# Kernel optimization log

Measured on AMD Instinct MI355X. Metric: run time of the kernel, lower is better.

The kernel has to match this reference:

```python
import jax, jax.numpy as jnp
import numpy as np

L = 2      # shared recursion blocks
B = 2
T = 4096
D = 1024
H = 16
DH = D // H
F = 4096
K = 2048   # token-choice capacity (active tokens per sequence)
S = 0.02   # init scale


def setup_inputs() -> dict:
    key = jax.random.key(0)
    ks = jax.random.split(key, 8)
    return {
        "x": jax.random.normal(ks[0], (B, T, D), jnp.float32),
        "router_w": jax.random.normal(ks[1], (D,), jnp.float32) * S,
        "router_b": jnp.zeros((), jnp.float32),
        "ln1_w": jnp.ones((L, D), jnp.float32),
        "ln1_b": jnp.zeros((L, D), jnp.float32),
        "wqkv": jax.random.normal(ks[2], (L, D, 3 * D), jnp.float32) * S,
        "wo": jax.random.normal(ks[3], (L, D, D), jnp.float32) * S,
        "ln2_w": jnp.ones((L, D), jnp.float32),
        "ln2_b": jnp.zeros((L, D), jnp.float32),
        "w1": jax.random.normal(ks[4], (L, D, F), jnp.float32) * S,
        "w2": jax.random.normal(ks[5], (L, F, D), jnp.float32) * S,
        "k": K,
    }


def _ln(x, w, b):
    mu = x.mean(-1, keepdims=True)
    var = ((x - mu) ** 2).mean(-1, keepdims=True)
    return (x - mu) * jax.lax.rsqrt(var + 1e-5) * w + b


def _block(h, ln1w, ln1b, wqkv, wo, ln2w, ln2b, w1, w2):
    # pre-LN MHA + pre-LN MLP transformer block over the active token subset
    Bk, Kk, Dd = h.shape
    y = _ln(h, ln1w, ln1b)
    qkv = jnp.einsum("bkd,de->bke", y, wqkv)          # [B,K,3D]
    q, kk, v = jnp.split(qkv, 3, axis=-1)
    sh = lambda t: t.reshape(Bk, Kk, H, DH).transpose(0, 2, 1, 3)  # [B,H,K,DH]
    q, kk, v = sh(q), sh(kk), sh(v)
    scores = jnp.einsum("bhqd,bhkd->bhqk", q, kk) / jnp.sqrt(jnp.float32(DH))
    att = jax.nn.softmax(scores, axis=-1)
    o = jnp.einsum("bhqk,bhkd->bhqd", att, v).transpose(0, 2, 1, 3).reshape(Bk, Kk, Dd)
    h = h + jnp.einsum("bkd,de->bke", o, wo)
    y = _ln(h, ln2w, ln2b)
    h = h + jnp.einsum("bkf,fd->bkd", jax.nn.gelu(jnp.einsum("bkd,df->bkf", y, w1)), w2)
    return h


def reference(x, router_w, router_b, ln1_w, ln1_b, wqkv, wo, ln2_w, ln2_b, w1, w2, k):
    # --- token-choice router: per-token scalar logit, top-k capacity selection ---
    logits = jnp.einsum("btd,d->bt", x, router_w) + router_b       # [B,T]
    top_v, selected = jax.lax.top_k(logits, k)                     # [B,K]
    gate_w = jax.nn.sigmoid(top_v)[..., None]                      # [B,K,1]
    # --- gather active tokens (torch.gather along dim 1) ---
    top_k_x = jnp.take_along_axis(x, selected[..., None], axis=1)  # [B,K,D]
    # --- shared recursion blocks ---
    h = top_k_x
    for l in range(L):
        h = _block(h, ln1_w[l], ln1_b[l], wqkv[l], wo[l],
                   ln2_w[l], ln2_b[l], w1[l], w2[l])
    h_out = h * gate_w                                             # weighted gating
    # --- scatter_add back into the full sequence ---
    b_idx = jnp.arange(x.shape[0])[:, None]                        # [B,1]
    out = x.at[b_idx, selected].add(h_out)
    return out
```

## Files before the change

### kernel.cpp

```cpp
#include <hip/hip_runtime.h>
#include <cmath>

typedef __bf16 bf16;
typedef __bf16 bf16x2 __attribute__((ext_vector_type(2)));
typedef __bf16 bf16x4 __attribute__((ext_vector_type(4)));
typedef __bf16 bf16x8 __attribute__((ext_vector_type(8)));
typedef float  f32x4  __attribute__((ext_vector_type(4)));

#define AS1(p) ((const __attribute__((address_space(1))) void*)(p))
#define AS3(p) ((__attribute__((address_space(3))) void*)(p))

constexpr int Bc = 2, Tc = 4096, Dc = 1024, Hc = 16, Fc = 4096, Kc = 2048;

__global__ __launch_bounds__(256) void router_kernel(const float* __restrict__ x,
    const float* __restrict__ rw, const float* __restrict__ rb, float* __restrict__ logits,
    int* __restrict__ slot, int* __restrict__ sel, float* __restrict__ gate){
  int flat = blockIdx.x * 256 + threadIdx.x;
  if (flat < Bc * Tc) slot[flat] = -1;
  if (flat < Bc * Kc){ sel[flat] = flat & (Kc - 1); gate[flat] = 0.f; }
  int wv = threadIdx.x >> 6, lane = threadIdx.x & 63;
  int token = blockIdx.x * 4 + wv;
  const float* xr = x + (size_t)token * Dc;
  float s = 0.f;
#pragma unroll
  for (int i = 0; i < 16; i++){ int d = lane + i*64; s += xr[d] * rw[d]; }
#pragma unroll
  for (int m = 32; m; m >>= 1) s += __shfl_xor(s, m);
  if (lane == 0) logits[token] = s + rb[0];
}

__global__ __launch_bounds__(256) void topk_kernel(const float* __restrict__ logits,
    int* __restrict__ slot, int* __restrict__ sel, float* __restrict__ gate){
  __shared__ float lg[Tc];
  int b = blockIdx.x >> 7, seg = blockIdx.x & 127;
  const float* lb = logits + (size_t)b * Tc;
#pragma unroll
  for (int i = 0; i < 4; i++)
    *(float4*)&lg[(threadIdx.x + i*256)*4] = *(const float4*)&lb[(threadIdx.x + i*256)*4];
  __syncthreads();
  int t = seg * 32 + (threadIdx.x >> 3);
  int c = threadIdx.x & 7;
  float v = lg[t];
  int rank = 0;
#pragma unroll 4
  for (int j4 = c*128; j4 < c*128 + 128; j4++){
    float4 u4 = *(const float4*)&lg[j4*4];
    int j = j4*4;
    rank += (u4.x > v) || (u4.x == v && (j+0) < t);
    rank += (u4.y > v) || (u4.y == v && (j+1) < t);
    rank += (u4.z > v) || (u4.z == v && (j+2) < t);
    rank += (u4.w > v) || (u4.w == v && (j+3) < t);
  }
  rank += __shfl_xor(rank, 1);
  rank += __shfl_xor(rank, 2);
  rank += __shfl_xor(rank, 4);
  if (c == 0 && rank < Kc){
    sel [b*Kc + rank] = t;
    gate[b*Kc + rank] = 1.f / (1.f + expf(-v));
    slot[b*Tc + t] = rank;
  }
}

__global__ __launch_bounds__(256) void gather_kernel(const float* __restrict__ x,
    const int* __restrict__ sel, float* __restrict__ h){
  int row = blockIdx.x;
  int b = row >> 11;
  int t = sel[row];
  t = (t < 0) ? 0 : (t >= Tc ? Tc - 1 : t);
  const float* xr = x + ((size_t)b * Tc + t) * Dc;
  float* hr = h + (size_t)row * Dc;
  int d = threadIdx.x * 4;
  *(float4*)(hr + d) = *(const float4*)(xr + d);
}

__global__ __launch_bounds__(256) void ln_kernel(const float* __restrict__ h,
    const float* __restrict__ w, const float* __restrict__ bb, bf16* __restrict__ y){
  __shared__ float red[4], red2[4];
  int row = blockIdx.x, t = threadIdx.x;
  int wv = t >> 6, lane = t & 63;
  const float* hr = h + (size_t)row * Dc;
  float4 x4 = *(const float4*)(hr + t*4);
  float s = x4.x + x4.y + x4.z + x4.w;
#pragma unroll
  for (int m = 32; m; m >>= 1) s += __shfl_xor(s, m);
  if (lane == 0) red[wv] = s;
  __syncthreads();
  float mu = (red[0]+red[1]+red[2]+red[3]) * (1.f/Dc);
  float d0 = x4.x-mu, d1 = x4.y-mu, d2 = x4.z-mu, d3 = x4.w-mu;
  float q = d0*d0 + d1*d1 + d2*d2 + d3*d3;
#pragma unroll
  for (int m = 32; m; m >>= 1) q += __shfl_xor(q, m);
  if (lane == 0) red2[wv] = q;
  __syncthreads();
  float var = (red2[0]+red2[1]+red2[2]+red2[3]) * (1.f/Dc);
  float rs = rsqrtf(var + 1e-5f);
  bf16* yr = y + (size_t)row * Dc;
  int d = t * 4;
  float xv[4] = {x4.x, x4.y, x4.z, x4.w};
#pragma unroll
  for (int i = 0; i < 4; i++)
    yr[d+i] = (bf16)((xv[i]-mu) * rs * w[d+i] + bb[d+i]);
}

__device__ __forceinline__ void transpose_tile(const float* __restrict__ in,
    bf16* __restrict__ out, int R, int C, int bx, int by, bf16 (*tile)[72]){
  int c0 = bx * 64, r0 = by * 64;
  int t = threadIdx.x;
#pragma unroll
  for (int i = 0; i < 2; i++){
    int ch = t + i*256;
    int row = ch >> 3, col8 = (ch & 7) * 8;
    const float* src = in + (size_t)(r0+row)*C + c0 + col8;
    float4 a = *(const float4*)src;
    float4 b = *(const float4*)(src + 4);
    bf16x8 v;
    v[0]=(bf16)a.x; v[1]=(bf16)a.y; v[2]=(bf16)a.z; v[3]=(bf16)a.w;
    v[4]=(bf16)b.x; v[5]=(bf16)b.y; v[6]=(bf16)b.z; v[7]=(bf16)b.w;
    *(bf16x8*)&tile[row][col8] = v;
  }
  __syncthreads();
#pragma unroll
  for (int i = 0; i < 2; i++){
    int ch = t + i*256;
    int orow = ch >> 3, oc8 = (ch & 7) * 8;
    bf16x8 v;
#pragma unroll
    for (int j = 0; j < 8; j++) v[j] = tile[oc8+j][orow];
    *(bf16x8*)(out + (size_t)(c0+orow)*R + r0 + oc8) = v;
  }
}

__global__ __launch_bounds__(256) void transpose4_kernel(
    const float* __restrict__ wqkv, const float* __restrict__ wo,
    const float* __restrict__ w1,   const float* __restrict__ w2,
    bf16* __restrict__ wqkvT, bf16* __restrict__ woT,
    bf16* __restrict__ w1T,   bf16* __restrict__ w2T){
  __shared__ __attribute__((aligned(16))) bf16 tile[64][72];
  int id = blockIdx.x;
  if (id < 768)        transpose_tile(wqkv, wqkvT, Dc, 3*Dc, id % 48,        id / 48,        tile);
  else if (id < 1024){ int t = id - 768;  transpose_tile(wo, woT, Dc, Dc,   t % 16,         t / 16,         tile); }
  else if (id < 2048){ int t = id - 1024; transpose_tile(w1, w1T, Dc, Fc,   t % 64,         t / 64,         tile); }
  else               { int t = id - 2048; transpose_tile(w2, w2T, Fc, Dc,   t % 16,         t / 16,         tile); }
}

__device__ __forceinline__ float fast_gelu(float v){
  float u = exp2f(v * (1.f + 0.044715f*v*v) * -2.30220772f);
  return v * __builtin_amdgcn_rcpf(1.f + u);
}

__global__ __launch_bounds__(256) void gemm_bt_kernel(
    const bf16* __restrict__ A, const bf16* __restrict__ Bt,
    bf16* __restrict__ Cbf, float* __restrict__ Cf,
    int M, int N, int Kd, int mode)
{
  __shared__ __attribute__((aligned(16))) bf16 As[128*64];
  __shared__ __attribute__((aligned(16))) bf16 Bs[128*64];
  const int tid = threadIdx.x;
  const int wv = tid >> 6, lane = tid & 63;
  const int wm = wv & 1, wn = wv >> 1;
  const int quad = lane >> 4, l15 = lane & 15;
  const int m0 = blockIdx.y * 128, n0 = blockIdx.x * 128;
  f32x4 acc[4][4] = {};

  const int arow = tid >> 3;
  const int acol = ((tid & 7) ^ (arow & 7)) * 8;
  const bf16* Ag = A  + (size_t)(m0 + arow) * Kd + acol;
  const bf16* Bg = Bt + (size_t)(n0 + arow) * Kd + acol;
  char* AsB = (char*)As;
  char* BsB = (char*)Bs;
  const size_t rstep = (size_t)32 * Kd;

  const bf16* Ab = As + (size_t)(wm*64 + l15) * 64;
  const bf16* Bb = Bs + (size_t)(wn*64 + l15) * 64;
  const int rx = l15 & 7;

  for (int k0 = 0; k0 < Kd; k0 += 64){
    __syncthreads();
#pragma unroll
    for (int i = 0; i < 4; i++){
      __builtin_amdgcn_global_load_lds(AS1(Ag + i*rstep + k0), AS3(AsB + i*4096 + wv*1024), 16, 0, 0);
      __builtin_amdgcn_global_load_lds(AS1(Bg + i*rstep + k0), AS3(BsB + i*4096 + wv*1024), 16, 0, 0);
    }
    __syncthreads();
#pragma unroll
    for (int s = 0; s < 2; s++){
      const int ax = ((s*4 + quad) ^ rx) * 8;
      bf16x8 af[4], bfr[4];
#pragma unroll
      for (int mt = 0; mt < 4; mt++) af[mt]  = *(const bf16x8*)(Ab + mt*1024 + ax);
#pragma unroll
      for (int nt = 0; nt < 4; nt++) bfr[nt] = *(const bf16x8*)(Bb + nt*1024 + ax);
#pragma unroll
      for (int mt = 0; mt < 4; mt++)
#pragma unroll
        for (int nt = 0; nt < 4; nt++)
          acc[mt][nt] = __builtin_amdgcn_mfma_f32_16x16x32_bf16(af[mt], bfr[nt], acc[mt][nt], 0, 0, 0);
    }
  }
#pragma unroll
  for (int mt = 0; mt < 4; mt++){
    int rr0 = m0 + wm*64 + mt*16 + (lane>>4)*4;
#pragma unroll
    for (int nt = 0; nt < 4; nt++){
      int cc = n0 + wn*64 + nt*16 + (lane&15);
#pragma unroll
      for (int r = 0; r < 4; r++){
        float v = acc[mt][nt][r];
        size_t idx = (size_t)(rr0 + r) * N + cc;
        if (mode == 0)      Cbf[idx] = (bf16)v;
        else if (mode == 1) Cf[idx] += v;
        else                Cbf[idx] = (bf16)fast_gelu(v);
      }
    }
  }
}

__global__ __launch_bounds__(256) void gemm_bt64_kernel(
    const bf16* __restrict__ A, const bf16* __restrict__ Bt,
    bf16* __restrict__ Cbf, float* __restrict__ Cf,
    int M, int N, int Kd, int mode,
    const float* __restrict__ xg, const int* __restrict__ sel,
    const float* __restrict__ gatep, float* __restrict__ outp)
{
  __shared__ __attribute__((aligned(16))) bf16 As[128*64];
  __shared__ __attribute__((aligned(16))) bf16 Bs[64*64];
  const int tid = threadIdx.x;
  const int wv = tid >> 6, lane = tid & 63;
  const int wm = wv >> 1, wn = wv & 1;
  const int quad = lane >> 4, l15 = lane & 15;
  const int m0 = blockIdx.y * 128, n0 = blockIdx.x * 64;
  f32x4 acc[4][2] = {};

  const int arow = tid >> 3;
  const int acol = ((tid & 7) ^ (arow & 7)) * 8;
  const bf16* Ag = A  + (size_t)(m0 + arow) * Kd + acol;
  const bf16* Bg = Bt + (size_t)(n0 + arow) * Kd + acol;
  char* AsB = (char*)As;
  char* BsB = (char*)Bs;
  const size_t rstep = (size_t)32 * Kd;

  const bf16* Ab = As + (size_t)(wm*64 + l15) * 64;
  const bf16* Bb = Bs + (size_t)(wn*32 + l15) * 64;
  const int rx = l15 & 7;

  for (int k0 = 0; k0 < Kd; k0 += 64){
    __syncthreads();
#pragma unroll
    for (int i = 0; i < 4; i++)
      __builtin_amdgcn_global_load_lds(AS1(Ag + i*rstep + k0), AS3(AsB + i*4096 + wv*1024), 16, 0, 0);
#pragma unroll
    for (int i = 0; i < 2; i++)
      __builtin_amdgcn_global_load_lds(AS1(Bg + i*rstep + k0), AS3(BsB + i*4096 + wv*1024), 16, 0, 0);
    __syncthreads();
#pragma unroll
    for (int s = 0; s < 2; s++){
      const int ax = ((s*4 + quad) ^ rx) * 8;
      bf16x8 af[4], bfr[2];
#pragma unroll
      for (int mt = 0; mt < 4; mt++) af[mt]  = *(const bf16x8*)(Ab + mt*1024 + ax);
#pragma unroll
      for (int nt = 0; nt < 2; nt++) bfr[nt] = *(const bf16x8*)(Bb + nt*1024 + ax);
#pragma unroll
      for (int mt = 0; mt < 4; mt++)
#pragma unroll
        for (int nt = 0; nt < 2; nt++)
          acc[mt][nt] = __builtin_amdgcn_mfma_f32_16x16x32_bf16(af[mt], bfr[nt], acc[mt][nt], 0, 0, 0);
    }
  }
  if (mode == 3){
#pragma unroll
    for (int mt = 0; mt < 4; mt++){
      int rr0 = m0 + wm*64 + mt*16 + quad*4;
#pragma unroll
      for (int r = 0; r < 4; r++){
        int row = rr0 + r;
        int bb = row >> 11;
        int t  = sel[row];
        t = (t < 0) ? 0 : (t >= Tc ? Tc - 1 : t);
        float g = gatep[row];
        const size_t obase = ((size_t)bb * Tc + t) * (size_t)Dc;
#pragma unroll
        for (int nt = 0; nt < 2; nt++){
          int cc = n0 + wn*32 + nt*16 + l15;
          float hv = Cf[(size_t)row * N + cc] + acc[mt][nt][r];
          outp[obase + cc] = xg[obase + cc] + g * hv;
        }
      }
    }
    return;
  }
#pragma unroll
  for (int mt = 0; mt < 4; mt++){
    int rr0 = m0 + wm*64 + mt*16 + (lane>>4)*4;
#pragma unroll
    for (int nt = 0; nt < 2; nt++){
      int cc = n0 + wn*32 + nt*16 + (lane&15);
#pragma unroll
      for (int r = 0; r < 4; r++){
        float v = acc[mt][nt][r];
        size_t idx = (size_t)(rr0 + r) * N + cc;
        if (mode == 0)      Cbf[idx] = (bf16)v;
        else if (mode == 1) Cf[idx] += v;
        else                Cbf[idx] = (bf16)fast_gelu(v);
      }
    }
  }
}

__global__ __launch_bounds__(256) void flash_kernel(const bf16* __restrict__ qkv, bf16* __restrict__ o){
  __shared__ __attribute__((aligned(16))) bf16 Ks[64][72];
  __shared__ __attribute__((aligned(16))) bf16 Vt[64*64];
  __shared__ __attribute__((aligned(16))) bf16 Pt[4][64][16];
  const int tid = threadIdx.x, wv = tid >> 6, lane = tid & 63;
  const int quad = lane >> 4, l15 = lane & 15;
  const int bid = blockIdx.x;
  const int qt = bid & 31, hh = (bid >> 5) & 15, b = bid >> 9;
  const int q0 = qt * 64;
  const size_t base = (size_t)b * Kc * (3*Dc);
  const float SC2 = 0.125f * 1.44269504f;

  const int sp8 = (tid & 7) * 8;
  const int kr0 = tid >> 3, kr1 = kr0 + 32;
  const int vr0 = (tid >> 3) * 2;
  const int vg = vr0 >> 3, vlo = vr0 & 7, vsw = sp8 >> 3;

  bf16x8 qf[2];
  {
    const bf16* qr = qkv + base + (size_t)(q0 + wv*16 + l15)*(3*Dc) + hh*64 + quad*8;
    qf[0] = *(const bf16x8*)(qr);
    qf[1] = *(const bf16x8*)(qr + 32);
  }

  const bf16* kp0 = qkv + base + (size_t)kr0*(3*Dc) +   Dc + hh*64 + sp8;
  const bf16* kp1 = qkv + base + (size_t)kr1*(3*Dc) +   Dc + hh*64 + sp8;
  const bf16* vp0 = qkv + base + (size_t)vr0*(3*Dc) + 2*Dc + hh*64 + sp8;
  const bf16* vp1 = vp0 + 3*Dc;
  bf16x8 kpre0 = *(const bf16x8*)kp0;
  bf16x8 kpre1 = *(const bf16x8*)kp1;
  bf16x8 vpre0 = *(const bf16x8*)vp0;
  bf16x8 vpre1 = *(const bf16x8*)vp1;
  const int TSTRIDE = 64 * 3 * Dc;

  bf16x8 onesf;
#pragma unroll
  for (int j = 0; j < 8; j++) onesf[j] = (bf16)(l15 == 0 ? 1.f : 0.f);

  f32x4 oacc[4] = {};
  f32x4 oacc5 = {};
  float mrow[4];
#pragma unroll
  for (int r = 0; r < 4; r++) mrow[r] = -1e30f;

  for (int kt = 0; kt < 32; kt++){
    __syncthreads();
    *(bf16x8*)&Ks[kr0][sp8] = kpre0;
    *(bf16x8*)&Ks[kr1][sp8] = kpre1;
#pragma unroll
    for (int j = 0; j < 8; j++){
      bf16x2 pr; pr[0] = vpre0[j]; pr[1] = vpre1[j];
      *(bf16x2*)&Vt[(sp8 + j)*64 + ((vg ^ j ^ vsw) << 3) + vlo] = pr;
    }
    __syncthreads();
    if (kt < 31){
      kp0 += TSTRIDE; kp1 += TSTRIDE; vp0 += TSTRIDE; vp1 += TSTRIDE;
      kpre0 = *(const bf16x8*)kp0;
      kpre1 = *(const bf16x8*)kp1;
      vpre0 = *(const bf16x8*)vp0;
      vpre1 = *(const bf16x8*)vp1;
    }
    f32x4 sacc[4] = {};
    __builtin_amdgcn_s_setprio(1);
#pragma unroll
    for (int nt = 0; nt < 4; nt++)
#pragma unroll
      for (int s = 0; s < 2; s++){
        bf16x8 kf = *(const bf16x8*)&Ks[nt*16 + l15][s*32 + quad*8];
        sacc[nt] = __builtin_amdgcn_mfma_f32_16x16x32_bf16(qf[s], kf, sacc[nt], 0, 0, 0);
      }
    __builtin_amdgcn_s_setprio(0);
    float lm[4];
#pragma unroll
    for (int r = 0; r < 4; r++)
      lm[r] = fmaxf(fmaxf(sacc[0][r], sacc[1][r]), fmaxf(sacc[2][r], sacc[3][r]));
    bool ok = true;
#pragma unroll
    for (int r = 0; r < 4; r++) ok = ok && (lm[r] * SC2 <= mrow[r] + 8.f);
    if (!__all((int)ok)){
#pragma unroll
      for (int r = 0; r < 4; r++){
        float mx = lm[r];
#pragma unroll
        for (int m = 1; m < 16; m <<= 1) mx = fmaxf(mx, __shfl_xor(mx, m));
        float nm = fmaxf(mrow[r], mx * SC2);
        float alpha = exp2f(mrow[r] - nm);
        mrow[r] = nm;
#pragma unroll
        for (int nt = 0; nt < 4; nt++) oacc[nt][r] *= alpha;
        oacc5[r] *= alpha;
      }
    }
#pragma unroll
    for (int nt = 0; nt < 4; nt++){
      bf16x4 w;
#pragma unroll
      for (int r = 0; r < 4; r++) w[r] = (bf16)exp2f(fmaf(sacc[nt][r], SC2, -mrow[r]));
      *(bf16x4*)&Pt[wv][nt*16 + l15][quad*4] = w;
    }
    bf16x8 pf[2];
    {
      bf16x4 t00, t01, t10, t11;
      const bf16* pr0 = &Pt[wv][     quad*8][l15];
      const bf16* pr1 = &Pt[wv][32 + quad*8][l15];
      asm volatile("ds_read_b64_tr_b16 %0, %1"            : "=v"(t00) : "v"(AS3(pr0)) : "memory");
      asm volatile("ds_read_b64_tr_b16 %0, %1 offset:128" : "=v"(t01) : "v"(AS3(pr0)) : "memory");
      asm volatile("ds_read_b64_tr_b16 %0, %1"            : "=v"(t10) : "v"(AS3(pr1)) : "memory");
      asm volatile("ds_read_b64_tr_b16 %0, %1 offset:128" : "=v"(t11) : "v"(AS3(pr1)) : "memory");
      asm volatile("s_waitcnt lgkmcnt(0)" ::: "memory");
      __builtin_amdgcn_sched_barrier(0);
#pragma unroll
      for (int j = 0; j < 4; j++){
        pf[0][j] = t00[j]; pf[0][j+4] = t01[j];
        pf[1][j] = t10[j]; pf[1][j+4] = t11[j];
      }
    }
    __builtin_amdgcn_s_setprio(1);
#pragma unroll
    for (int nt = 0; nt < 4; nt++){
      int d = nt*16 + l15;
      int sw = (d & 7) ^ ((d >> 3) & 7);
#pragma unroll
      for (int s = 0; s < 2; s++){
        bf16x8 vf = *(const bf16x8*)&Vt[d*64 + (((s*4 + quad) ^ sw) << 3)];
        oacc[nt] = __builtin_amdgcn_mfma_f32_16x16x32_bf16(pf[s], vf, oacc[nt], 0, 0, 0);
      }
    }
    oacc5 = __builtin_amdgcn_mfma_f32_16x16x32_bf16(pf[0], onesf, oacc5, 0, 0, 0);
    oacc5 = __builtin_amdgcn_mfma_f32_16x16x32_bf16(pf[1], onesf, oacc5, 0, 0, 0);
    __builtin_amdgcn_s_setprio(0);
  }
#pragma unroll
  for (int r = 0; r < 4; r++){
    float l = __shfl(oacc5[r], lane & 48);
    float inv = __builtin_amdgcn_rcpf(l);
    int row = q0 + wv*16 + quad*4 + r;
#pragma unroll
    for (int nt = 0; nt < 4; nt++)
      o[((size_t)b*Kc + row)*Dc + hh*64 + nt*16 + l15] = (bf16)(oacc[nt][r] * inv);
  }
}

__global__ __launch_bounds__(256) void scatter_kernel(const float* __restrict__ x,
    const int* __restrict__ slot, float* __restrict__ out){
  int row = blockIdx.x;
  int sl = slot[row];
  if (sl >= 0 && sl < Kc) return;
  int d = threadIdx.x * 4;
  const float* xr = x + (size_t)row * Dc;
  float* orow = out + (size_t)row * Dc;
  *(float4*)(orow + d) = *(const float4*)(xr + d);
}

extern "C" void kernel_launch(void* const* d_in, const int* in_sizes, int n_in,
                              void* d_out, int out_size, void* d_ws, size_t ws_size,
                              hipStream_t stream)
{
  const float* x        = (const float*)d_in[0];
  const float* router_w = (const float*)d_in[1];
  const float* router_b = (const float*)d_in[2];
  const float* ln1_w    = (const float*)d_in[3];
  const float* ln1_b    = (const float*)d_in[4];
  const float* wqkv     = (const float*)d_in[5];
  const float* wo       = (const float*)d_in[6];
  const float* ln2_w    = (const float*)d_in[7];
  const float* ln2_b    = (const float*)d_in[8];
  const float* w1       = (const float*)d_in[9];
  const float* w2       = (const float*)d_in[10];
  float* out = (float*)d_out;

  char* ws = (char*)d_ws;
  if (ws_size < 84029440u) return;
  float* logits = (float*)(ws + 0);
  int*   slot   = (int*)  (ws + 36864);
  int*   sel    = (int*)  (ws + 73728);
  float* gate   = (float*)(ws + 94208);
  float* h      = (float*)(ws + 114688);
  bf16*  y      = (bf16*) (ws + 16896000);
  bf16*  big    = (bf16*) (ws + 25288704);
  bf16*  wqkvT  = (bf16*) (ws + 58847232);
  bf16*  woT    = (bf16*) (ws + 65142784);
  bf16*  w1T    = (bf16*) (ws + 67244032);
  bf16*  w2T    = (bf16*) (ws + 75636736);

  router_kernel<<<2048, 256, 0, stream>>>(x, router_w, router_b, logits, slot, sel, gate);
  topk_kernel<<<256, 256, 0, stream>>>(logits, slot, sel, gate);
  gather_kernel<<<4096, 256, 0, stream>>>(x, sel, h);

  for (int l = 0; l < 2; l++){
    transpose4_kernel<<<3072, 256, 0, stream>>>(
        wqkv + (size_t)l*Dc*3*Dc, wo + (size_t)l*Dc*Dc,
        w1 + (size_t)l*Dc*Fc,     w2 + (size_t)l*Fc*Dc,
        wqkvT, woT, w1T, w2T);

    ln_kernel<<<4096, 256, 0, stream>>>(h, ln1_w + l*Dc, ln1_b + l*Dc, y);
    gemm_bt_kernel<<<dim3(24,32), 256, 0, stream>>>(y, wqkvT, big, nullptr, 4096, 3*Dc, Dc, 0);
    flash_kernel<<<1024, 256, 0, stream>>>(big, y);
    gemm_bt64_kernel<<<dim3(16,32), 256, 0, stream>>>(y, woT, nullptr, h, 4096, Dc, Dc, 1,
                                                      nullptr, nullptr, nullptr, nullptr);
    ln_kernel<<<4096, 256, 0, stream>>>(h, ln2_w + l*Dc, ln2_b + l*Dc, y);
    gemm_bt_kernel<<<dim3(32,32), 256, 0, stream>>>(y, w1T, big, nullptr, 4096, Fc, Dc, 2);
    if (l == 0)
      gemm_bt64_kernel<<<dim3(16,32), 256, 0, stream>>>(big, w2T, nullptr, h, 4096, Dc, Fc, 1,
                                                        nullptr, nullptr, nullptr, nullptr);
    else
      gemm_bt64_kernel<<<dim3(16,32), 256, 0, stream>>>(big, w2T, nullptr, h, 4096, Dc, Fc, 3,
                                                        x, sel, gate, out);
  }

  scatter_kernel<<<8192, 256, 0, stream>>>(x, slot, out);
}
```

Before: 793.0 us.

## Double flash-attention KV tile to 128 and XCD-swizzle GEMM block order

The flash attention kernel now processes 128 keys per iteration instead of 64, with larger K, V-transposed and P shared-memory tiles. This halves the number of loop iterations and block-wide barriers and gives more MFMA work per synchronisation, at the cost of more LDS and registers per block, which may lower occupancy. Both GEMM kernels remap block IDs with an XCD-aware swizzle so that neighbouring tiles run on the same XCD and share its L2.

```diff
diff --git a/kernel.cpp b/kernel.cpp
--- a/kernel.cpp
+++ b/kernel.cpp
@@ -148,6 +148,10 @@
   return v * __builtin_amdgcn_rcpf(1.f + u);
 }
 
+__device__ __forceinline__ int xcd_swizzle(int id, int nwg){
+  return (id & 7) * (nwg >> 3) + (id >> 3);
+}
+
 __global__ __launch_bounds__(256) void gemm_bt_kernel(
     const bf16* __restrict__ A, const bf16* __restrict__ Bt,
     bf16* __restrict__ Cbf, float* __restrict__ Cf,
@@ -159,7 +163,9 @@
   const int wv = tid >> 6, lane = tid & 63;
   const int wm = wv & 1, wn = wv >> 1;
   const int quad = lane >> 4, l15 = lane & 15;
-  const int m0 = blockIdx.y * 128, n0 = blockIdx.x * 128;
+  const int nwg = gridDim.x * gridDim.y;
+  const int bid = xcd_swizzle(blockIdx.y * gridDim.x + blockIdx.x, nwg);
+  const int m0 = (bid / gridDim.x) * 128, n0 = (bid % gridDim.x) * 128;
   f32x4 acc[4][4] = {};
 
   const int arow = tid >> 3;
@@ -228,7 +234,9 @@
   const int wv = tid >> 6, lane = tid & 63;
   const int wm = wv >> 1, wn = wv & 1;
   const int quad = lane >> 4, l15 = lane & 15;
-  const int m0 = blockIdx.y * 128, n0 = blockIdx.x * 64;
+  const int nwg = gridDim.x * gridDim.y;
+  const int bid = xcd_swizzle(blockIdx.y * gridDim.x + blockIdx.x, nwg);
+  const int m0 = (bid / gridDim.x) * 128, n0 = (bid % gridDim.x) * 64;
   f32x4 acc[4][2] = {};
 
   const int arow = tid >> 3;
@@ -308,9 +316,9 @@
 }
 
 __global__ __launch_bounds__(256) void flash_kernel(const bf16* __restrict__ qkv, bf16* __restrict__ o){
-  __shared__ __attribute__((aligned(16))) bf16 Ks[64][72];
-  __shared__ __attribute__((aligned(16))) bf16 Vt[64*64];
-  __shared__ __attribute__((aligned(16))) bf16 Pt[4][64][16];
+  __shared__ __attribute__((aligned(16))) bf16 Ks[128][72];
+  __shared__ __attribute__((aligned(16))) bf16 Vt[128*64];
+  __shared__ __attribute__((aligned(16))) bf16 Pt[4][128][16];
   const int tid = threadIdx.x, wv = tid >> 6, lane = tid & 63;
   const int quad = lane >> 4, l15 = lane & 15;
   const int bid = blockIdx.x;
@@ -320,7 +328,7 @@
   const float SC2 = 0.125f * 1.44269504f;
 
   const int sp8 = (tid & 7) * 8;
-  const int kr0 = tid >> 3, kr1 = kr0 + 32;
+  const int kr0 = tid >> 3;
   const int vr0 = (tid >> 3) * 2;
   const int vg = vr0 >> 3, vlo = vr0 & 7, vsw = sp8 >> 3;
 
@@ -331,15 +339,18 @@
     qf[1] = *(const bf16x8*)(qr + 32);
   }
 
-  const bf16* kp0 = qkv + base + (size_t)kr0*(3*Dc) +   Dc + hh*64 + sp8;
-  const bf16* kp1 = qkv + base + (size_t)kr1*(3*Dc) +   Dc + hh*64 + sp8;
-  const bf16* vp0 = qkv + base + (size_t)vr0*(3*Dc) + 2*Dc + hh*64 + sp8;
-  const bf16* vp1 = vp0 + 3*Dc;
-  bf16x8 kpre0 = *(const bf16x8*)kp0;
-  bf16x8 kpre1 = *(const bf16x8*)kp1;
-  bf16x8 vpre0 = *(const bf16x8*)vp0;
-  bf16x8 vpre1 = *(const bf16x8*)vp1;
-  const int TSTRIDE = 64 * 3 * Dc;
+  const bf16* kp[4]; const bf16* vp[4];
+#pragma unroll
+  for (int i = 0; i < 4; i++)
+    kp[i] = qkv + base + (size_t)(kr0 + i*32)*(3*Dc) + Dc + hh*64 + sp8;
+  vp[0] = qkv + base + (size_t)(vr0     )*(3*Dc) + 2*Dc + hh*64 + sp8;
+  vp[1] = vp[0] + 3*Dc;
+  vp[2] = qkv + base + (size_t)(vr0 + 64)*(3*Dc) + 2*Dc + hh*64 + sp8;
+  vp[3] = vp[2] + 3*Dc;
+  bf16x8 kpre[4], vpre[4];
+#pragma unroll
+  for (int i = 0; i < 4; i++){ kpre[i] = *(const bf16x8*)kp[i]; vpre[i] = *(const bf16x8*)vp[i]; }
+  const int TSTRIDE = 128 * 3 * Dc;
 
   bf16x8 onesf;
 #pragma unroll
@@ -351,27 +362,31 @@
 #pragma unroll
   for (int r = 0; r < 4; r++) mrow[r] = -1e30f;
 
-  for (int kt = 0; kt < 32; kt++){
+  for (int kt = 0; kt < 16; kt++){
     __syncthreads();
-    *(bf16x8*)&Ks[kr0][sp8] = kpre0;
-    *(bf16x8*)&Ks[kr1][sp8] = kpre1;
+#pragma unroll
+    for (int i = 0; i < 4; i++)
+      *(bf16x8*)&Ks[kr0 + i*32][sp8] = kpre[i];
 #pragma unroll
     for (int j = 0; j < 8; j++){
-      bf16x2 pr; pr[0] = vpre0[j]; pr[1] = vpre1[j];
-      *(bf16x2*)&Vt[(sp8 + j)*64 + ((vg ^ j ^ vsw) << 3) + vlo] = pr;
+      bf16x2 pa; pa[0] = vpre[0][j]; pa[1] = vpre[1][j];
+      bf16x2 pb; pb[0] = vpre[2][j]; pb[1] = vpre[3][j];
+      *(bf16x2*)&Vt[(sp8 + j)*128 + (((vg    ) ^ j ^ vsw) << 3) + vlo] = pa;
+      *(bf16x2*)&Vt[(sp8 + j)*128 + (((vg + 8) ^ j ^ vsw) << 3) + vlo] = pb;
     }
     __syncthreads();
-    if (kt < 31){
-      kp0 += TSTRIDE; kp1 += TSTRIDE; vp0 += TSTRIDE; vp1 += TSTRIDE;
-      kpre0 = *(const bf16x8*)kp0;
-      kpre1 = *(const bf16x8*)kp1;
-      vpre0 = *(const bf16x8*)vp0;
-      vpre1 = *(const bf16x8*)vp1;
-    }
-    f32x4 sacc[4] = {};
+    if (kt < 15){
+#pragma unroll
+      for (int i = 0; i < 4; i++){
+        kp[i] += TSTRIDE; vp[i] += TSTRIDE;
+        kpre[i] = *(const bf16x8*)kp[i];
+        vpre[i] = *(const bf16x8*)vp[i];
+      }
+    }
+    f32x4 sacc[8] = {};
     __builtin_amdgcn_s_setprio(1);
 #pragma unroll
-    for (int nt = 0; nt < 4; nt++)
+    for (int nt = 0; nt < 8; nt++)
 #pragma unroll
       for (int s = 0; s < 2; s++){
         bf16x8 kf = *(const bf16x8*)&Ks[nt*16 + l15][s*32 + quad*8];
@@ -380,8 +395,11 @@
     __builtin_amdgcn_s_setprio(0);
     float lm[4];
 #pragma unroll
-    for (int r = 0; r < 4; r++)
-      lm[r] = fmaxf(fmaxf(sacc[0][r], sacc[1][r]), fmaxf(sacc[2][r], sacc[3][r]));
+    for (int r = 0; r < 4; r++){
+      float m0 = fmaxf(fmaxf(sacc[0][r], sacc[1][r]), fmaxf(sacc[2][r], sacc[3][r]));
+      float m1 = fmaxf(fmaxf(sacc[4][r], sacc[5][r]), fmaxf(sacc[6][r], sacc[7][r]));
+      lm[r] = fmaxf(m0, m1);
+    }
     bool ok = true;
 #pragma unroll
     for (int r = 0; r < 4; r++) ok = ok && (lm[r] * SC2 <= mrow[r] + 8.f);
@@ -400,28 +418,29 @@
       }
     }
 #pragma unroll
-    for (int nt = 0; nt < 4; nt++){
+    for (int nt = 0; nt < 8; nt++){
       bf16x4 w;
 #pragma unroll
       for (int r = 0; r < 4; r++) w[r] = (bf16)exp2f(fmaf(sacc[nt][r], SC2, -mrow[r]));
       *(bf16x4*)&Pt[wv][nt*16 + l15][quad*4] = w;
     }
-    bf16x8 pf[2];
+    bf16x8 pf[4];
     {
-      bf16x4 t00, t01, t10, t11;
-      const bf16* pr0 = &Pt[wv][     quad*8][l15];
-      const bf16* pr1 = &Pt[wv][32 + quad*8][l15];
-      asm volatile("ds_read_b64_tr_b16 %0, %1"            : "=v"(t00) : "v"(AS3(pr0)) : "memory");
-      asm volatile("ds_read_b64_tr_b16 %0, %1 offset:128" : "=v"(t01) : "v"(AS3(pr0)) : "memory");
-      asm volatile("ds_read_b64_tr_b16 %0, %1"            : "=v"(t10) : "v"(AS3(pr1)) : "memory");
-      asm volatile("ds_read_b64_tr_b16 %0, %1 offset:128" : "=v"(t11) : "v"(AS3(pr1)) : "memory");
+      bf16x4 tlo[4], thi[4];
+#pragma unroll
+      for (int s = 0; s < 4; s++){
+        const bf16* pr = &Pt[wv][s*32 + quad*8][l15];
+        asm volatile("ds_read_b64_tr_b16 %0, %1"            : "=v"(tlo[s]) : "v"(AS3(pr)) : "memory");
+        asm volatile("ds_read_b64_tr_b16 %0, %1 offset:128" : "=v"(thi[s]) : "v"(AS3(pr)) : "memory");
+      }
       asm volatile("s_waitcnt lgkmcnt(0)" ::: "memory");
       __builtin_amdgcn_sched_barrier(0);
 #pragma unroll
-      for (int j = 0; j < 4; j++){
-        pf[0][j] = t00[j]; pf[0][j+4] = t01[j];
-        pf[1][j] = t10[j]; pf[1][j+4] = t11[j];
-      }
+      for (int s = 0; s < 4; s++)
+#pragma unroll
+        for (int j = 0; j < 4; j++){
+          pf[s][j] = tlo[s][j]; pf[s][j+4] = thi[s][j];
+        }
     }
     __builtin_amdgcn_s_setprio(1);
 #pragma unroll
@@ -429,13 +448,14 @@
       int d = nt*16 + l15;
       int sw = (d & 7) ^ ((d >> 3) & 7);
 #pragma unroll
-      for (int s = 0; s < 2; s++){
-        bf16x8 vf = *(const bf16x8*)&Vt[d*64 + (((s*4 + quad) ^ sw) << 3)];
+      for (int s = 0; s < 4; s++){
+        bf16x8 vf = *(const bf16x8*)&Vt[d*128 + (((s*4 + quad) ^ sw) << 3)];
         oacc[nt] = __builtin_amdgcn_mfma_f32_16x16x32_bf16(pf[s], vf, oacc[nt], 0, 0, 0);
       }
     }
-    oacc5 = __builtin_amdgcn_mfma_f32_16x16x32_bf16(pf[0], onesf, oacc5, 0, 0, 0);
-    oacc5 = __builtin_amdgcn_mfma_f32_16x16x32_bf16(pf[1], onesf, oacc5, 0, 0, 0);
+#pragma unroll
+    for (int s = 0; s < 4; s++)
+      oacc5 = __builtin_amdgcn_mfma_f32_16x16x32_bf16(pf[s], onesf, oacc5, 0, 0, 0);
     __builtin_amdgcn_s_setprio(0);
   }
 #pragma unroll
```

After: 800.6 us. About the same (+1.0%).
